# Kernel tuning notes

Hardware: AMD Instinct MI355X
Metric: run time of the kernel (lower is better)

Reference implementation:

```python
import jax, jax.numpy as jnp
import numpy as np

B, T, TQ, D, S = 32, 4096, 64, 256, 64
L = T // S  # span length (contiguous, non-overlapping spans covering the doc)


def setup_inputs() -> dict:
    key = jax.random.key(0)
    k1, k2, k3, k4 = jax.random.split(key, 4)
    document_encoded = jax.random.normal(k1, (B, T, D), dtype=jnp.float32)
    query_encoded = jax.random.normal(k2, (B, TQ, D), dtype=jnp.float32)
    # variable document lengths in [T//2, T]
    lengths = jax.random.randint(k3, (B,), T // 2, T + 1)
    document_mask = (jnp.arange(T)[None, :] < lengths[:, None]).astype(jnp.float32)
    starts = jnp.arange(S, dtype=jnp.int64) * L
    spans = jnp.broadcast_to(jnp.stack([starts, starts + L], axis=-1), (B, S, 2))
    sentence_scores = jax.random.uniform(k4, (B, S), dtype=jnp.float32)
    return {
        "document_encoded": document_encoded,
        "query_encoded": query_encoded,
        "document_mask": document_mask,
        "spans": spans,
        "sentence_scores": sentence_scores,
    }


def softmax_mask(scores, mask):
    # Faithful translation of ASReader.softmax_mask
    masked = scores * mask
    shifted = (masked - jnp.max(masked, axis=1, keepdims=True)) * mask
    logdenom = jnp.log(jnp.sum(jnp.exp(shifted) * mask, axis=1, keepdims=True))
    logprobs = (shifted - logdenom) * mask
    return jnp.exp(logprobs) * mask


def adjust_scores(probs, spans, sentence_scores):
    # probs: [B,T]; spans: [B,S,2]; sentence_scores: [B,S]
    t = jnp.arange(probs.shape[1])  # [T]
    memb = ((t[None, None, :] >= spans[..., 0:1]) &
            (t[None, None, :] < spans[..., 1:2])).astype(probs.dtype)  # [B,S,T]
    count = jnp.sum(memb, axis=-1)                                   # [B,S]
    span_sum = jnp.einsum("bst,bt->bs", memb, probs)                  # [B,S]
    span_mean = span_sum / jnp.maximum(count, 1)
    nz = span_mean != 0
    scale = jnp.where(nz, sentence_scores / jnp.where(nz, span_mean, 1.0), 1.0)
    covered = jnp.sum(memb, axis=1)                                   # [B,T] (0/1, spans disjoint)
    token_scale = jnp.einsum("bst,bs->bt", memb, scale) + (1.0 - covered)
    probs = probs * token_scale
    return probs / jnp.sum(probs, axis=1, keepdims=True)


def reference(document_encoded, query_encoded, document_mask, spans, sentence_scores):
    # F.max_pool1d with kernel_size = full query length == max over query tokens
    query_pooled = jnp.max(query_encoded, axis=1)                     # [B,D]
    scores = jnp.einsum("btd,bd->bt", document_encoded, query_pooled)  # [B,T]
    probs = softmax_mask(scores, document_mask)
    return adjust_scores(probs, spans, sentence_scores)
```

## Files before the change

### kernel.cpp

```cpp
#include <hip/hip_runtime.h>
#include <math.h>
#include <float.h>

namespace {

constexpr int kB  = 32;
constexpr int kT  = 4096;
constexpr int kTQ = 64;
constexpr int kD  = 256;
constexpr int kS  = 64;

__global__ __launch_bounds__(1024) void qpool_kernel(const float* __restrict__ q,
                                                     float* __restrict__ qp) {
  const int b = blockIdx.x;
  const int tid = threadIdx.x;
  const int d = tid & 255;
  const int g = tid >> 8;
  const float* base = q + ((size_t)b * kTQ + g * 16) * kD + d;
  float m = base[0];
#pragma unroll
  for (int tq = 1; tq < 16; ++tq) m = fmaxf(m, base[tq * kD]);
  __shared__ float red[4][kD];
  red[g][d] = m;
  __syncthreads();
  if (g == 0) {
    qp[b * kD + d] = fmaxf(fmaxf(red[0][d], red[1][d]), fmaxf(red[2][d], red[3][d]));
  }
}

__global__ __launch_bounds__(256) void span_kernel(const float* __restrict__ doc,
                                                   const float* __restrict__ mask,
                                                   const float* __restrict__ qp,
                                                   float* __restrict__ P,
                                                   float* __restrict__ stm,
                                                   float* __restrict__ stse) {
  const int blk = blockIdx.x;
  const int b = blk >> 6;
  const int wave = threadIdx.x >> 6;
  const int lane = threadIdx.x & 63;
  const int t0 = blk * 64 + wave * 16;

  const float4 qv = reinterpret_cast<const float4*>(qp + b * kD)[lane];
  const float* dbase = doc + (size_t)t0 * kD + lane * 4;

  float myv = 0.f;
#pragma unroll
  for (int i = 0; i < 16; ++i) {
    const float4 dv = *reinterpret_cast<const float4*>(dbase + (size_t)i * kD);
    float s = (dv.x * qv.x + dv.y * qv.y) + (dv.z * qv.z + dv.w * qv.w);
#pragma unroll
    for (int off = 32; off >= 1; off >>= 1) s += __shfl_xor(s, off, 64);
    if (lane == i) myv = s;
  }

  const float mk = (lane < 16) ? mask[t0 + lane] : 0.f;
  const float v = (mk != 0.f) ? myv : -INFINITY;

  float wm = v;
#pragma unroll
  for (int off = 32; off >= 1; off >>= 1) wm = fmaxf(wm, __shfl_xor(wm, off, 64));
  __shared__ float smax[4], ssum[4];
  if (lane == 0) smax[wave] = wm;
  __syncthreads();
  const float m_s = fmaxf(fmaxf(smax[0], smax[1]), fmaxf(smax[2], smax[3]));

  const float e = (v == -INFINITY) ? 0.f : expf(v - m_s);
  float ws = e;
#pragma unroll
  for (int off = 32; off >= 1; off >>= 1) ws += __shfl_xor(ws, off, 64);
  if (lane == 0) ssum[wave] = ws;
  __syncthreads();

  if (lane < 16) P[t0 + lane] = e;
  if (threadIdx.x == 0) {
    stm[blk] = m_s;
    stse[blk] = (ssum[0] + ssum[1]) + (ssum[2] + ssum[3]);
  }
}

__global__ __launch_bounds__(256) void fin_kernel(const float* __restrict__ sscore,
                                                  const float* __restrict__ stm,
                                                  const float* __restrict__ stse,
                                                  float* __restrict__ out) {
  const int blk = blockIdx.x;
  const int b = blk >> 2;
  const int qtr = blk & 3;
  const int tid = threadIdx.x;
  __shared__ float wbuf[kS];

  if (tid < kS) {
    const float m = stm[b * kS + tid];
    const float se = stse[b * kS + tid];
    const bool mv = se > 0.f;
    float g = mv ? m : -INFINITY;
#pragma unroll
    for (int off = 32; off >= 1; off >>= 1) g = fmaxf(g, __shfl_xor(g, off, 64));
    float contrib = mv ? expf(m - g) * se : 0.f;
    float den = contrib;
#pragma unroll
    for (int off = 32; off >= 1; off >>= 1) den += __shfl_xor(den, off, 64);
    const float logden = logf(den);

    const float t1 = mv ? expf((m - g) - logden) : 0.f;
    const float span_sum = t1 * se;
    const float sm = span_sum * (1.f / 64.f);
    const bool alive = mv && (sm >= FLT_MIN);

    const float s0 = sscore[b * kS + tid];
    float ssv = alive ? s0 : 0.f;
#pragma unroll
    for (int off = 32; off >= 1; off >>= 1) ssv += __shfl_xor(ssv, off, 64);
    wbuf[tid] = alive ? s0 / (se * ssv) : 0.f;
  }
  __syncthreads();

  float* op = out + (size_t)b * kT;
  const int i4 = qtr * 256 + tid;
  float4 p = reinterpret_cast<float4*>(op)[i4];
  const float w = wbuf[i4 >> 4];
  p.x *= w; p.y *= w; p.z *= w; p.w *= w;
  reinterpret_cast<float4*>(op)[i4] = p;
}

}

extern "C" void kernel_launch(void* const* d_in, const int* in_sizes, int n_in,
                              void* d_out, int out_size, void* d_ws, size_t ws_size,
                              hipStream_t stream) {
  const float* doc    = (const float*)d_in[0];
  const float* q      = (const float*)d_in[1];
  const float* mask   = (const float*)d_in[2];
  const float* sscore = (const float*)d_in[4];
  float* out = (float*)d_out;

  float* qp   = (float*)d_ws;
  float* stm  = qp + kB * kD;
  float* stse = stm + kB * kS;

  qpool_kernel<<<kB, 1024, 0, stream>>>(q, qp);
  span_kernel<<<kB * kS, 256, 0, stream>>>(doc, mask, qp, out, stm, stse);
  fin_kernel<<<kB * 4, 256, 0, stream>>>(sscore, stm, stse, out);
}
```

Before: 34.11 us.

## Assign 4 lanes per token in span dot product and split qpool blocks

The span kernel's dot product changes from one token per wave iteration, which used a full 64-lane shuffle reduction per token, to 4 lanes per token that each accumulate over strided quarters of D. Only a 2-step shuffle is then needed. The pooled query is staged in shared memory and kept in registers. The query-pool kernel is split into 4 blocks per batch of 256 threads to raise parallelism. The cost is more registers per thread and a strided doc access pattern, where each 4-lane group reads 64 contiguous bytes per load.

Measured after the change: 32.82 us. -3.8%, faster.

```diff
diff --git a/kernel.cpp b/kernel.cpp
--- a/kernel.cpp
+++ b/kernel.cpp
@@ -10,21 +10,25 @@
 constexpr int kD  = 256;
 constexpr int kS  = 64;
 
-__global__ __launch_bounds__(1024) void qpool_kernel(const float* __restrict__ q,
-                                                     float* __restrict__ qp) {
-  const int b = blockIdx.x;
+__global__ __launch_bounds__(256) void qpool_kernel(const float* __restrict__ q,
+                                                    float* __restrict__ qp) {
+  const int blk = blockIdx.x;
+  const int b = blk >> 2;
+  const int dg = blk & 3;
   const int tid = threadIdx.x;
-  const int d = tid & 255;
-  const int g = tid >> 8;
+  const int dd = tid & 63;
+  const int g = tid >> 6;
+  const int d = dg * 64 + dd;
   const float* base = q + ((size_t)b * kTQ + g * 16) * kD + d;
   float m = base[0];
 #pragma unroll
   for (int tq = 1; tq < 16; ++tq) m = fmaxf(m, base[tq * kD]);
-  __shared__ float red[4][kD];
-  red[g][d] = m;
+  __shared__ float red[4][64];
+  red[g][dd] = m;
   __syncthreads();
   if (g == 0) {
-    qp[b * kD + d] = fmaxf(fmaxf(red[0][d], red[1][d]), fmaxf(red[2][d], red[3][d]));
+    qp[b * kD + d] =
+        fmaxf(fmaxf(red[0][dd], red[1][dd]), fmaxf(red[2][dd], red[3][dd]));
   }
 }
 
@@ -36,25 +40,42 @@
                                                    float* __restrict__ stse) {
   const int blk = blockIdx.x;
   const int b = blk >> 6;
-  const int wave = threadIdx.x >> 6;
-  const int lane = threadIdx.x & 63;
-  const int t0 = blk * 64 + wave * 16;
+  const int tid = threadIdx.x;
+  const int wave = tid >> 6;
+  const int lane = tid & 63;
 
-  const float4 qv = reinterpret_cast<const float4*>(qp + b * kD)[lane];
-  const float* dbase = doc + (size_t)t0 * kD + lane * 4;
+  __shared__ float qpl[kD];
+  qpl[tid] = qp[b * kD + tid];
+  __syncthreads();
 
-  float myv = 0.f;
+  float4 qv[16];
 #pragma unroll
-  for (int i = 0; i < 16; ++i) {
-    const float4 dv = *reinterpret_cast<const float4*>(dbase + (size_t)i * kD);
-    float s = (dv.x * qv.x + dv.y * qv.y) + (dv.z * qv.z + dv.w * qv.w);
-#pragma unroll
-    for (int off = 32; off >= 1; off >>= 1) s += __shfl_xor(s, off, 64);
-    if (lane == i) myv = s;
+  for (int it = 0; it < 16; ++it) {
+    qv[it] = *reinterpret_cast<const float4*>(&qpl[(lane & 3) * 4 + it * 16]);
   }
 
-  const float mk = (lane < 16) ? mask[t0 + lane] : 0.f;
-  const float v = (mk != 0.f) ? myv : -INFINITY;
+  const int myTok = lane >> 2;
+  const int t0 = blk * 64 + wave * 16;
+  const float* dbase = doc + (size_t)(t0 + myTok) * kD + (lane & 3) * 4;
+
+  float a0 = 0.f, a1 = 0.f, a2 = 0.f, a3 = 0.f;
+#pragma unroll
+  for (int it = 0; it < 16; it += 4) {
+    const float4 d0 = *reinterpret_cast<const float4*>(dbase + (it + 0) * 16);
+    const float4 d1 = *reinterpret_cast<const float4*>(dbase + (it + 1) * 16);
+    const float4 d2 = *reinterpret_cast<const float4*>(dbase + (it + 2) * 16);
+    const float4 d3 = *reinterpret_cast<const float4*>(dbase + (it + 3) * 16);
+    a0 += d0.x * qv[it + 0].x + d0.y * qv[it + 0].y + d0.z * qv[it + 0].z + d0.w * qv[it + 0].w;
+    a1 += d1.x * qv[it + 1].x + d1.y * qv[it + 1].y + d1.z * qv[it + 1].z + d1.w * qv[it + 1].w;
+    a2 += d2.x * qv[it + 2].x + d2.y * qv[it + 2].y + d2.z * qv[it + 2].z + d2.w * qv[it + 2].w;
+    a3 += d3.x * qv[it + 3].x + d3.y * qv[it + 3].y + d3.z * qv[it + 3].z + d3.w * qv[it + 3].w;
+  }
+  float acc = (a0 + a1) + (a2 + a3);
+  acc += __shfl_xor(acc, 1, 64);
+  acc += __shfl_xor(acc, 2, 64);
+
+  const float mk = mask[t0 + myTok];
+  const float v = (mk != 0.f) ? acc : -INFINITY;
 
   float wm = v;
 #pragma unroll
@@ -68,11 +89,11 @@
   float ws = e;
 #pragma unroll
   for (int off = 32; off >= 1; off >>= 1) ws += __shfl_xor(ws, off, 64);
-  if (lane == 0) ssum[wave] = ws;
+  if (lane == 0) ssum[wave] = ws * 0.25f;
   __syncthreads();
 
-  if (lane < 16) P[t0 + lane] = e;
-  if (threadIdx.x == 0) {
+  if ((lane & 3) == 0) P[t0 + myTok] = e;
+  if (tid == 0) {
     stm[blk] = m_s;
     stse[blk] = (ssum[0] + ssum[1]) + (ssum[2] + ssum[3]);
   }
@@ -137,7 +158,7 @@
   float* stm  = qp + kB * kD;
   float* stse = stm + kB * kS;
 
-  qpool_kernel<<<kB, 1024, 0, stream>>>(q, qp);
+  qpool_kernel<<<kB * 4, 256, 0, stream>>>(q, qp);
   span_kernel<<<kB * kS, 256, 0, stream>>>(doc, mask, qp, out, stm, stse);
   fin_kernel<<<kB * 4, 256, 0, stream>>>(sscore, stm, stse, out);
 }
```
